# Performance work log

Hardware: AMD Instinct MI355X
Metric: run time of the kernel (lower is better)

Reference implementation:

```python
import jax, jax.numpy as jnp
import numpy as np

NUM_LEVELS = 12
LEVEL_DIM = 2
BASE_RES = 16
DESIRED_RES = 8192
LOG2_HASH = 21
PRIMES = (1, 2654435761, 805459861)


def _level_specs(D):
    # torch-ngp GridEncoder table layout: per-level (offset, size, scale, res, use_hash)
    f = (DESIRED_RES / BASE_RES) ** (1.0 / (NUM_LEVELS - 1))
    specs = []
    offset = 0
    for l in range(NUM_LEVELS):
        scale = BASE_RES * (f ** l) - 1.0
        res = int(np.ceil(scale)) + 1
        dense = (res + 1) ** D  # align_corners=False -> stride uses res+1
        params = min(2 ** LOG2_HASH, dense)
        params = int(np.ceil(params / 8) * 8)
        specs.append((offset, params, scale, res, dense > 2 ** LOG2_HASH))
        offset += params
    return specs, offset


def grid_encode(x, table, D):
    # x: [N, D] in [-1, 1]; table: [T, LEVEL_DIM]. Returns [N, NUM_LEVELS*LEVEL_DIM].
    x01 = (x + 1.0) * 0.5  # (inputs + bound) / (2*bound), bound=1
    specs, _ = _level_specs(D)
    feats = []
    for (off, hsize, scale, res, use_hash) in specs:
        pos = x01 * scale + 0.5  # align_corners=False
        pg_f = jnp.floor(pos)
        frac = pos - pg_f          # [N, D]
        pg = pg_f.astype(jnp.uint32)
        acc = jnp.zeros((x.shape[0], LEVEL_DIM), dtype=table.dtype)
        for c in range(2 ** D):  # 4 or 8 corners, static unroll
            w = None
            idx = jnp.zeros((x.shape[0],), dtype=jnp.uint32)
            stride = 1
            for d in range(D):
                bit = (c >> d) & 1
                coord = pg[:, d] + jnp.uint32(bit)
                wd = frac[:, d] if bit else (1.0 - frac[:, d])
                w = wd if w is None else w * wd
                if use_hash:
                    idx = idx ^ (coord * jnp.uint32(PRIMES[d]))  # uint32 wraparound xor-hash
                else:
                    idx = idx + coord * jnp.uint32(stride)
                    stride *= (res + 1)
            gidx = (idx % jnp.uint32(hsize)).astype(jnp.int32) + off
            acc = acc + w[:, None] * table[gidx]
        feats.append(acc)
    return jnp.concatenate(feats, axis=-1)


def mlp(feat, w1, b1, w2, b2):
    h = jax.nn.relu(feat @ w1 + b1)
    return h @ w2 + b2


def setup_inputs() -> dict:
    key = jax.random.key(0)
    ks = jax.random.split(key, 16)
    B, P = 4096, 1000
    line = jax.random.uniform(ks[0], (B, 2), dtype=jnp.float32)
    line_points = jax.random.uniform(ks[1], (B, P, 3), dtype=jnp.float32)
    gt_o = jax.random.uniform(ks[2], (B, P), dtype=jnp.float32)
    _, tot2 = _level_specs(2)
    _, tot3 = _level_specs(3)
    table_conf = jax.random.uniform(ks[3], (tot2, LEVEL_DIM), jnp.float32, -1e-4, 1e-4)
    table_op = jax.random.uniform(ks[4], (tot3, LEVEL_DIM), jnp.float32, -1e-4, 1e-4)
    F = NUM_LEVELS * LEVEL_DIM  # 24
    w1_c = jax.random.normal(ks[5], (F, 64), jnp.float32) * 0.1
    b1_c = jnp.zeros((64,), jnp.float32)
    w2_c = jax.random.normal(ks[6], (64, 1), jnp.float32) * 0.1
    b2_c = jnp.zeros((1,), jnp.float32)
    w1_o = jax.random.normal(ks[7], (F, 64), jnp.float32) * 0.1
    b1_o = jnp.zeros((64,), jnp.float32)
    w2_o = jax.random.normal(ks[8], (64, 1), jnp.float32) * 0.1
    b2_o = jnp.zeros((1,), jnp.float32)
    return {"line": line, "line_points": line_points, "gt_o": gt_o,
            "table_conf": table_conf, "w1_c": w1_c, "b1_c": b1_c, "w2_c": w2_c, "b2_c": b2_c,
            "table_op": table_op, "w1_o": w1_o, "b1_o": b1_o, "w2_o": w2_o, "b2_o": b2_o}


def reference(line, line_points, gt_o, table_conf, w1_c, b1_c, w2_c, b2_c,
              table_op, w1_o, b1_o, w2_o, b2_o):
    B, P, _ = line_points.shape
    pts = line_points.reshape(B * P, 3)
    feat_o = grid_encode(pts, table_op, 3)             # [B*P, 24]
    opacity = mlp(feat_o, w1_o, b1_o, w2_o, b2_o).reshape(B, P)  # squeeze(2)
    feat_c = grid_encode(line, table_conf, 2)          # [B, 24]
    confidence = mlp(feat_c, w1_c, b1_c, w2_c, b2_c)[:, 0]       # squeeze(1)
    loss1 = jnp.abs(opacity - gt_o)
    col_w = jnp.where(jnp.arange(P) < 500, 4.0 / 3.0, 2.0 / 3.0).astype(loss1.dtype)
    loss1 = loss1 * col_w[None, :]
    loss = jnp.exp(-confidence) * loss1.mean(axis=1) + confidence
    return loss.mean()
```

## Files before the change

kernel.cpp:

```cpp
#include <hip/hip_runtime.h>
#include <hip/hip_bf16.h>
#include <math.h>

#define NLEV 12
#define B_LINES 4096
#define P_PTS 1000
#define FP8_SCALE 65536.0f
#define FP8_ISCALE (1.0f / 65536.0f)

typedef unsigned short ushort_t;
typedef __attribute__((ext_vector_type(8))) short short8_t;
typedef __attribute__((ext_vector_type(4))) float f32x4;

struct LevelSpec {
    unsigned off;
    unsigned mask;
    float    scale;
    unsigned R;
};
struct Specs { LevelSpec L[NLEV]; };
struct HashScales { float s[8]; };

static unsigned compute_specs(int D, Specs* sp) {
    double f = pow(8192.0 / 16.0, 1.0 / 11.0);
    unsigned offset = 0;
    for (int l = 0; l < NLEV; ++l) {
        double scale = 16.0 * pow(f, (double)l) - 1.0;
        int res = (int)ceil(scale) + 1;
        unsigned long long dense = 1ull;
        for (int d = 0; d < D; ++d) dense *= (unsigned long long)(res + 1);
        unsigned long long params = dense > (1ull << 21) ? (1ull << 21) : dense;
        params = ((params + 7ull) / 8ull) * 8ull;
        sp->L[l].off   = offset;
        sp->L[l].mask  = (unsigned)params - 1u;
        sp->L[l].scale = (float)scale;
        sp->L[l].R     = (unsigned)(res + 1);
        offset += (unsigned)params;
    }
    return offset;
}


__device__ __forceinline__ float block_reduce_256(float v) {
    __shared__ float red[256];
    int tid = threadIdx.x;
    red[tid] = v;
    __syncthreads();
    #pragma unroll
    for (int s = 128; s >= 1; s >>= 1) {
        if (tid < s) red[tid] += red[tid + s];
        __syncthreads();
    }
    return red[0];
}

__device__ __forceinline__ unsigned short f32_to_bf16_bits(float f) {
    unsigned u = __float_as_uint(f);
    unsigned r = (u + 0x7fffu + ((u >> 16) & 1u)) >> 16;
    return (unsigned short)r;
}

__device__ __forceinline__ float mlp_24_64_1(const float feat[24],
        const float* __restrict__ w1, const float* __restrict__ b1,
        const float* __restrict__ w2, const float* __restrict__ b2) {
    float o = b2[0];
    #pragma unroll
    for (int half = 0; half < 2; ++half) {
        float h[32];
        #pragma unroll
        for (int j = 0; j < 32; ++j) h[j] = b1[half * 32 + j];
        #pragma unroll
        for (int k = 0; k < 24; ++k) {
            float fv = feat[k];
            #pragma unroll
            for (int j = 0; j < 32; ++j)
                h[j] = fmaf(fv, w1[k * 64 + half * 32 + j], h[j]);
        }
        #pragma unroll
        for (int j = 0; j < 32; ++j)
            o = fmaf(fmaxf(h[j], 0.f), w2[half * 32 + j], o);
    }
    return o;
}

__global__ void __launch_bounds__(256) convert_kernel(
        const float2* __restrict__ in, ushort_t* __restrict__ out, int n) {
    int i = blockIdx.x * 256 + threadIdx.x;
    if (i >= n) return;
    float2 v = in[i];
    int p = __builtin_amdgcn_cvt_pk_fp8_f32(v.x * FP8_SCALE, v.y * FP8_SCALE,
                                            0, false);
    out[i] = (ushort_t)(p & 0xffff);
}

__global__ void __launch_bounds__(256) enc_dense_kernel(
        const float* __restrict__ pts, int pbase, int npts,
        const ushort_t* __restrict__ tabq,
        __hip_bfloat162* __restrict__ feats,
        Specs sp) {
    int i = blockIdx.x * 256 + threadIdx.x;
    if (i >= npts) return;
    int gp = pbase + i;
    float x0 = (pts[3 * gp + 0] + 1.f) * 0.5f;
    float x1 = (pts[3 * gp + 1] + 1.f) * 0.5f;
    float x2 = (pts[3 * gp + 2] + 1.f) * 0.5f;
    #pragma unroll
    for (int l = 0; l < 4; ++l) {
        const LevelSpec L = sp.L[l];
        float p0 = x0 * L.scale + 0.5f;
        float p1 = x1 * L.scale + 0.5f;
        float p2 = x2 * L.scale + 0.5f;
        float f0 = floorf(p0), f1 = floorf(p1), f2 = floorf(p2);
        float r0 = p0 - f0, r1 = p1 - f1, r2 = p2 - f2;
        float u0 = 1.f - r0, u1 = 1.f - r1, u2 = 1.f - r2;
        unsigned g0 = (unsigned)f0, g1 = (unsigned)f1, g2 = (unsigned)f2;
        const ushort_t* __restrict__ base = tabq + L.off;
        unsigned R = L.R, R2 = R * R;
        unsigned y0 = g1 * R, y1 = y0 + R;
        unsigned z0 = g2 * R2, z1 = z0 + R2;
        int t[8];
        #pragma unroll
        for (int c = 0; c < 8; ++c) {
            unsigned idx = (g0 + ((c & 1) ? 1u : 0u))
                         + ((c & 2) ? y1 : y0) + ((c & 4) ? z1 : z0);
            t[c] = (int)base[idx];
        }
        float a0 = 0.f, a1 = 0.f;
        #pragma unroll
        for (int c = 0; c < 8; ++c) {
            float w = ((c & 1) ? r0 : u0) * ((c & 2) ? r1 : u1)
                    * ((c & 4) ? r2 : u2);
            a0 = fmaf(w, __builtin_amdgcn_cvt_f32_fp8(t[c], 0), a0);
            a1 = fmaf(w, __builtin_amdgcn_cvt_f32_fp8(t[c], 1), a1);
        }
        __hip_bfloat162 o;
        o.x = __float2bfloat16(a0 * FP8_ISCALE);
        o.y = __float2bfloat16(a1 * FP8_ISCALE);
        feats[(size_t)l * npts + i] = o;
    }
}

__global__ void __launch_bounds__(256) enc_hash_all_kernel(
        const float* __restrict__ pts, int pbase, int npts,
        const ushort_t* __restrict__ tabq, unsigned hash_off0,
        HashScales hs,
        __hip_bfloat162* __restrict__ feats) {
    const int lev = blockIdx.x & 7;
    const int i = (blockIdx.x >> 3) * 256 + threadIdx.x;
    if (i >= npts) return;
    float scale = hs.s[0];
    #pragma unroll
    for (int k = 1; k < 8; ++k) if (lev == k) scale = hs.s[k];
    const ushort_t* __restrict__ base =
        tabq + hash_off0 + ((unsigned)lev << 21);
    const unsigned m = (1u << 21) - 1u;

    int gp = pbase + i;
    float x0 = (pts[3 * gp + 0] + 1.f) * 0.5f;
    float x1 = (pts[3 * gp + 1] + 1.f) * 0.5f;
    float x2 = (pts[3 * gp + 2] + 1.f) * 0.5f;
    float p0 = x0 * scale + 0.5f;
    float p1 = x1 * scale + 0.5f;
    float p2 = x2 * scale + 0.5f;
    float f0 = floorf(p0), f1 = floorf(p1), f2 = floorf(p2);
    float r0 = p0 - f0, r1 = p1 - f1, r2 = p2 - f2;
    float u0 = 1.f - r0, u1 = 1.f - r1, u2 = 1.f - r2;
    unsigned g0 = (unsigned)f0, g1 = (unsigned)f1, g2 = (unsigned)f2;
    unsigned y0 = g1 * 2654435761u, y1 = y0 + 2654435761u;
    unsigned z0 = g2 * 805459861u,  z1 = z0 + 805459861u;
    int t[8];
    #pragma unroll
    for (int c = 0; c < 8; ++c) {
        unsigned h = (g0 + ((c & 1) ? 1u : 0u))
                   ^ ((c & 2) ? y1 : y0) ^ ((c & 4) ? z1 : z0);
        t[c] = (int)base[h & m];
    }
    float a0 = 0.f, a1 = 0.f;
    #pragma unroll
    for (int c = 0; c < 8; ++c) {
        float w = ((c & 1) ? r0 : u0) * ((c & 2) ? r1 : u1)
                * ((c & 4) ? r2 : u2);
        a0 = fmaf(w, __builtin_amdgcn_cvt_f32_fp8(t[c], 0), a0);
        a1 = fmaf(w, __builtin_amdgcn_cvt_f32_fp8(t[c], 1), a1);
    }
    __hip_bfloat162 o;
    o.x = __float2bfloat16(a0 * FP8_ISCALE);
    o.y = __float2bfloat16(a1 * FP8_ISCALE);
    feats[(size_t)(4 + lev) * npts + i] = o;
}

__global__ void __launch_bounds__(256) mlp_loss_mfma_kernel(
        const unsigned* __restrict__ feats, int npts,
        const float* __restrict__ gt, int line0,
        const float* __restrict__ w1, const float* __restrict__ b1,
        const float* __restrict__ w2, const float* __restrict__ b2,
        float* __restrict__ S) {
    const int line_local = blockIdx.x;
    const int tid  = threadIdx.x;
    const int wave = tid >> 6;
    const int lane = tid & 63;
    const int c = lane & 15;
    const int g = lane >> 4;

    short8_t bfrag[4];
    #pragma unroll
    for (int nb = 0; nb < 4; ++nb) {
        #pragma unroll
        for (int i = 0; i < 8; ++i) {
            int k = g * 8 + i;
            float v = (k < 24) ? w1[k * 64 + nb * 16 + c] : 0.f;
            bfrag[nb][i] = (short)f32_to_bf16_bits(v);
        }
    }
    float b1v[4], w2v[4];
    #pragma unroll
    for (int nb = 0; nb < 4; ++nb) {
        b1v[nb] = b1[nb * 16 + c];
        w2v[nb] = w2[nb * 16 + c];
    }
    const float b2v = b2[0];

    const size_t lbase = (size_t)line_local * P_PTS;
    float lsum = 0.f;

    for (int it = 0; it < 16; ++it) {
        const int base16 = it * 64 + wave * 16;
        int prow = base16 + c;
        int pcl  = prow < P_PTS ? prow : P_PTS - 1;
        size_t pidx = lbase + (size_t)pcl;
        union { unsigned u[4]; short8_t v; } a;
        if (g < 3) {
            #pragma unroll
            for (int s = 0; s < 4; ++s)
                a.u[s] = feats[(size_t)(g * 4 + s) * npts + pidx];
        } else {
            a.u[0] = 0u; a.u[1] = 0u; a.u[2] = 0u; a.u[3] = 0u;
        }
        f32x4 acc[4];
        #pragma unroll
        for (int nb = 0; nb < 4; ++nb) {
            f32x4 ci = {b1v[nb], b1v[nb], b1v[nb], b1v[nb]};
            acc[nb] = __builtin_amdgcn_mfma_f32_16x16x32_bf16(
                a.v, bfrag[nb], ci, 0, 0, 0);
        }
        float part[4];
        #pragma unroll
        for (int r = 0; r < 4; ++r) {
            float s = fmaxf(acc[0][r], 0.f) * w2v[0];
            s = fmaf(fmaxf(acc[1][r], 0.f), w2v[1], s);
            s = fmaf(fmaxf(acc[2][r], 0.f), w2v[2], s);
            s = fmaf(fmaxf(acc[3][r], 0.f), w2v[3], s);
            part[r] = s;
        }
        #pragma unroll
        for (int off = 1; off < 16; off <<= 1) {
            #pragma unroll
            for (int r = 0; r < 4; ++r)
                part[r] += __shfl_xor(part[r], off);
        }
        if (c < 4) {
            int p = base16 + g * 4 + c;
            if (p < P_PTS) {
                float op = part[c] + b2v;
                float gv = gt[(size_t)(line0 + line_local) * P_PTS + p];
                float cw = (p < 500) ? (float)(4.0 / 3.0) : (float)(2.0 / 3.0);
                lsum += fabsf(op - gv) * cw;
            }
        }
    }
    float tot = block_reduce_256(lsum);
    if (tid == 0) S[line0 + line_local] = tot;
}

__global__ void __launch_bounds__(256) opacity_mono_kernel(
        const float* __restrict__ pts, const float* __restrict__ gt,
        const float2* __restrict__ tab,
        const float* __restrict__ w1, const float* __restrict__ b1,
        const float* __restrict__ w2, const float* __restrict__ b2,
        float* __restrict__ S, Specs sp) {
    const int b = blockIdx.x;
    const int tid = threadIdx.x;
    float lsum = 0.f;
    for (int p = tid; p < P_PTS; p += 256) {
        const int i = b * P_PTS + p;
        float x0 = (pts[3 * i + 0] + 1.f) * 0.5f;
        float x1 = (pts[3 * i + 1] + 1.f) * 0.5f;
        float x2 = (pts[3 * i + 2] + 1.f) * 0.5f;
        float feat[24];
        #pragma unroll
        for (int l = 0; l < NLEV; ++l) {
            const LevelSpec L = sp.L[l];
            float p0 = x0 * L.scale + 0.5f;
            float p1 = x1 * L.scale + 0.5f;
            float p2 = x2 * L.scale + 0.5f;
            float f0 = floorf(p0), f1 = floorf(p1), f2 = floorf(p2);
            float r0 = p0 - f0, r1 = p1 - f1, r2 = p2 - f2;
            float u0 = 1.f - r0, u1 = 1.f - r1, u2 = 1.f - r2;
            unsigned g0 = (unsigned)f0, g1 = (unsigned)f1, g2 = (unsigned)f2;
            float a0 = 0.f, a1 = 0.f;
            if (l >= 4) {
                unsigned y0 = g1 * 2654435761u, y1 = y0 + 2654435761u;
                unsigned z0 = g2 * 805459861u,  z1 = z0 + 805459861u;
                unsigned m = L.mask;
                #pragma unroll
                for (int c = 0; c < 8; ++c) {
                    unsigned h = (g0 + ((c & 1) ? 1u : 0u))
                               ^ ((c & 2) ? y1 : y0) ^ ((c & 4) ? z1 : z0);
                    float2 t = tab[L.off + (h & m)];
                    float w = ((c & 1) ? r0 : u0) * ((c & 2) ? r1 : u1)
                            * ((c & 4) ? r2 : u2);
                    a0 = fmaf(w, t.x, a0); a1 = fmaf(w, t.y, a1);
                }
            } else {
                unsigned R = L.R, R2 = R * R;
                unsigned y0 = g1 * R, y1 = y0 + R;
                unsigned z0 = g2 * R2, z1 = z0 + R2;
                #pragma unroll
                for (int c = 0; c < 8; ++c) {
                    unsigned idx = (g0 + ((c & 1) ? 1u : 0u))
                                 + ((c & 2) ? y1 : y0) + ((c & 4) ? z1 : z0);
                    float2 t = tab[L.off + idx];
                    float w = ((c & 1) ? r0 : u0) * ((c & 2) ? r1 : u1)
                            * ((c & 4) ? r2 : u2);
                    a0 = fmaf(w, t.x, a0); a1 = fmaf(w, t.y, a1);
                }
            }
            feat[2 * l] = a0; feat[2 * l + 1] = a1;
        }
        float op = mlp_24_64_1(feat, w1, b1, w2, b2);
        float cw = (p < 500) ? (float)(4.0 / 3.0) : (float)(2.0 / 3.0);
        lsum += fabsf(op - gt[i]) * cw;
    }
    float tot = block_reduce_256(lsum);
    if (tid == 0) S[b] = tot;
}

__global__ void __launch_bounds__(256) conf_kernel(
        const float* __restrict__ line, const float2* __restrict__ tab,
        const float* __restrict__ w1, const float* __restrict__ b1,
        const float* __restrict__ w2, const float* __restrict__ b2,
        const float* __restrict__ S, float* __restrict__ partial, Specs sp) {
    const int b = blockIdx.x * 256 + threadIdx.x;
    float x0 = (line[2 * b + 0] + 1.f) * 0.5f;
    float x1 = (line[2 * b + 1] + 1.f) * 0.5f;
    float feat[24];
    #pragma unroll
    for (int l = 0; l < NLEV; ++l) {
        const unsigned off = sp.L[l].off;
        const float scale = sp.L[l].scale;
        float p0 = x0 * scale + 0.5f;
        float p1 = x1 * scale + 0.5f;
        float f0 = floorf(p0), f1 = floorf(p1);
        float r0 = p0 - f0, r1 = p1 - f1;
        float u0 = 1.f - r0, u1 = 1.f - r1;
        unsigned g0 = (unsigned)f0, g1 = (unsigned)f1;
        unsigned idx0, idx1, idx2, idx3;
        if (l >= 8) {
            const unsigned mask = sp.L[l].mask;
            unsigned a1 = g1 * 2654435761u, bb1 = a1 + 2654435761u;
            idx0 = (g0 ^ a1) & mask;
            idx1 = ((g0 + 1u) ^ a1) & mask;
            idx2 = (g0 ^ bb1) & mask;
            idx3 = ((g0 + 1u) ^ bb1) & mask;
        } else {
            const unsigned R = sp.L[l].R;
            unsigned a1 = g1 * R, bb1 = a1 + R;
            idx0 = g0 + a1; idx1 = g0 + 1u + a1;
            idx2 = g0 + bb1; idx3 = g0 + 1u + bb1;
        }
        float2 t0 = tab[off + idx0], t1 = tab[off + idx1];
        float2 t2 = tab[off + idx2], t3 = tab[off + idx3];
        float w0 = u0 * u1, w1c = r0 * u1, w2c = u0 * r1, w3 = r0 * r1;
        feat[2 * l]     = w0 * t0.x + w1c * t1.x + w2c * t2.x + w3 * t3.x;
        feat[2 * l + 1] = w0 * t0.y + w1c * t1.y + w2c * t2.y + w3 * t3.y;
    }
    float conf = mlp_24_64_1(feat, w1, b1, w2, b2);
    float term = expf(-conf) * (S[b] * (1.0f / (float)P_PTS)) + conf;
    float tot = block_reduce_256(term);
    if (threadIdx.x == 0) partial[blockIdx.x] = tot;
}

__global__ void final_kernel(const float* __restrict__ partial,
                             float* __restrict__ out) {
    if (threadIdx.x == 0) {
        float s = 0.f;
        for (int i = 0; i < 16; ++i) s += partial[i];
        out[0] = s * (1.0f / (float)B_LINES);
    }
}


extern "C" void kernel_launch(void* const* d_in, const int* in_sizes, int n_in,
                              void* d_out, int out_size, void* d_ws, size_t ws_size,
                              hipStream_t stream) {
    const float* line    = (const float*)d_in[0];
    const float* pts     = (const float*)d_in[1];
    const float* gt      = (const float*)d_in[2];
    const float* table_c = (const float*)d_in[3];
    const float* w1_c    = (const float*)d_in[4];
    const float* b1_c    = (const float*)d_in[5];
    const float* w2_c    = (const float*)d_in[6];
    const float* b2_c    = (const float*)d_in[7];
    const float* table_o = (const float*)d_in[8];
    const float* w1_o    = (const float*)d_in[9];
    const float* b1_o    = (const float*)d_in[10];
    const float* w2_o    = (const float*)d_in[11];
    const float* b2_o    = (const float*)d_in[12];
    (void)in_sizes; (void)n_in; (void)out_size;

    Specs sp3, sp2;
    unsigned tot3 = compute_specs(3, &sp3);
    compute_specs(2, &sp2);

    size_t tabB = (((size_t)tot3 * 2) + 255) & ~(size_t)255;
    size_t head = tabB + (size_t)B_LINES * 4 + 64;
    head = (head + 63) & ~(size_t)63;
    long max_lines = 0;
    if (ws_size > head + 64)
        max_lines = (long)((ws_size - head - 64) / ((size_t)P_PTS * 12 * 4));

    float* S       = (float*)((char*)d_ws + tabB);
    float* partial = S + B_LINES;

    if (max_lines >= 64) {
        ushort_t* tabq = (ushort_t*)d_ws;
        __hip_bfloat162* featbuf = (__hip_bfloat162*)((char*)d_ws + head);

        int chunk_lines = (int)(max_lines < B_LINES ? max_lines : B_LINES);
        int nch = (B_LINES + chunk_lines - 1) / chunk_lines;

        HashScales hs;
        for (int k = 0; k < 8; ++k) hs.s[k] = sp3.L[4 + k].scale;
        const unsigned hash_off0 = sp3.L[4].off;

        convert_kernel<<<((int)tot3 + 255) / 256, 256, 0, stream>>>(
            (const float2*)table_o, tabq, (int)tot3);

        for (int ch = 0; ch < nch; ++ch) {
            int line0 = ch * chunk_lines;
            int lines = B_LINES - line0 < chunk_lines ? B_LINES - line0
                                                      : chunk_lines;
            int npts = lines * P_PTS;
            int pbase = line0 * P_PTS;
            int nblk = (npts + 255) / 256;
            enc_dense_kernel<<<nblk, 256, 0, stream>>>(
                pts, pbase, npts, tabq, featbuf, sp3);
            enc_hash_all_kernel<<<nblk * 8, 256, 0, stream>>>(
                pts, pbase, npts, tabq, hash_off0, hs, featbuf);
            mlp_loss_mfma_kernel<<<lines, 256, 0, stream>>>(
                (const unsigned*)featbuf, npts, gt, line0,
                w1_o, b1_o, w2_o, b2_o, S);
        }
    } else {
        opacity_mono_kernel<<<B_LINES, 256, 0, stream>>>(
            pts, gt, (const float2*)table_o, w1_o, b1_o, w2_o, b2_o, S, sp3);
    }

    conf_kernel<<<16, 256, 0, stream>>>(
        line, (const float2*)table_c, w1_c, b1_c, w2_c, b2_c, S, partial, sp2);
    final_kernel<<<1, 64, 0, stream>>>(partial, (float*)d_out);
}
```

Before: 1.577 ms.

## Use persistent grid-stride hash encoding with two points per thread and nontemporal I/O

The hash-level encoder now launches a fixed 256 blocks per level and grid-strides over points. Each thread processes two points per iteration and issues all 16 table gathers before interpolating, which raises memory-level parallelism. Streaming loads of points and the fp32 table, and stores of features and the fp8 table, switch to nontemporal hints so they pollute the cache less and leave room for the random table gathers. Clamped indices for out-of-range tail points add some redundant work, and the fixed grid size may underfill or overfill the GPU depending on chunk size.

```diff
diff --git a/kernel.cpp b/kernel.cpp
--- a/kernel.cpp
+++ b/kernel.cpp
@@ -7,6 +7,7 @@
 #define P_PTS 1000
 #define FP8_SCALE 65536.0f
 #define FP8_ISCALE (1.0f / 65536.0f)
+#define NBLK_PER_LEV 256
 
 typedef unsigned short ushort_t;
 typedef __attribute__((ext_vector_type(8))) short short8_t;
@@ -60,6 +61,14 @@
     return (unsigned short)r;
 }
 
+__device__ __forceinline__ void store_nt_feat(__hip_bfloat162* p,
+                                              float a0, float a1) {
+    union { __hip_bfloat162 b; unsigned u; } cv;
+    cv.b.x = __float2bfloat16(a0 * FP8_ISCALE);
+    cv.b.y = __float2bfloat16(a1 * FP8_ISCALE);
+    __builtin_nontemporal_store(cv.u, (unsigned*)p);
+}
+
 __device__ __forceinline__ float mlp_24_64_1(const float feat[24],
         const float* __restrict__ w1, const float* __restrict__ b1,
         const float* __restrict__ w2, const float* __restrict__ b2) {
@@ -87,10 +96,12 @@
         const float2* __restrict__ in, ushort_t* __restrict__ out, int n) {
     int i = blockIdx.x * 256 + threadIdx.x;
     if (i >= n) return;
-    float2 v = in[i];
+    float2 v;
+    v.x = __builtin_nontemporal_load(&in[i].x);
+    v.y = __builtin_nontemporal_load(&in[i].y);
     int p = __builtin_amdgcn_cvt_pk_fp8_f32(v.x * FP8_SCALE, v.y * FP8_SCALE,
                                             0, false);
-    out[i] = (ushort_t)(p & 0xffff);
+    __builtin_nontemporal_store((ushort_t)(p & 0xffff), &out[i]);
 }
 
 __global__ void __launch_bounds__(256) enc_dense_kernel(
@@ -101,9 +112,9 @@
     int i = blockIdx.x * 256 + threadIdx.x;
     if (i >= npts) return;
     int gp = pbase + i;
-    float x0 = (pts[3 * gp + 0] + 1.f) * 0.5f;
-    float x1 = (pts[3 * gp + 1] + 1.f) * 0.5f;
-    float x2 = (pts[3 * gp + 2] + 1.f) * 0.5f;
+    float x0 = (__builtin_nontemporal_load(pts + 3 * gp + 0) + 1.f) * 0.5f;
+    float x1 = (__builtin_nontemporal_load(pts + 3 * gp + 1) + 1.f) * 0.5f;
+    float x2 = (__builtin_nontemporal_load(pts + 3 * gp + 2) + 1.f) * 0.5f;
     #pragma unroll
     for (int l = 0; l < 4; ++l) {
         const LevelSpec L = sp.L[l];
@@ -133,11 +144,47 @@
             a0 = fmaf(w, __builtin_amdgcn_cvt_f32_fp8(t[c], 0), a0);
             a1 = fmaf(w, __builtin_amdgcn_cvt_f32_fp8(t[c], 1), a1);
         }
-        __hip_bfloat162 o;
-        o.x = __float2bfloat16(a0 * FP8_ISCALE);
-        o.y = __float2bfloat16(a1 * FP8_ISCALE);
-        feats[(size_t)l * npts + i] = o;
-    }
+        store_nt_feat(&feats[(size_t)l * npts + i], a0, a1);
+    }
+}
+
+struct HashPt { unsigned h[8]; float r0, r1, r2; };
+
+__device__ __forceinline__ HashPt hash_addrs(
+        const float* __restrict__ pts, int gp, float scale, unsigned m) {
+    float x0 = (__builtin_nontemporal_load(pts + 3 * gp + 0) + 1.f) * 0.5f;
+    float x1 = (__builtin_nontemporal_load(pts + 3 * gp + 1) + 1.f) * 0.5f;
+    float x2 = (__builtin_nontemporal_load(pts + 3 * gp + 2) + 1.f) * 0.5f;
+    float p0 = x0 * scale + 0.5f;
+    float p1 = x1 * scale + 0.5f;
+    float p2 = x2 * scale + 0.5f;
+    float f0 = floorf(p0), f1 = floorf(p1), f2 = floorf(p2);
+    HashPt o;
+    o.r0 = p0 - f0; o.r1 = p1 - f1; o.r2 = p2 - f2;
+    unsigned g0 = (unsigned)f0, g1 = (unsigned)f1, g2 = (unsigned)f2;
+    unsigned y0 = g1 * 2654435761u, y1 = y0 + 2654435761u;
+    unsigned z0 = g2 * 805459861u,  z1 = z0 + 805459861u;
+    #pragma unroll
+    for (int c = 0; c < 8; ++c) {
+        unsigned h = (g0 + ((c & 1) ? 1u : 0u))
+                   ^ ((c & 2) ? y1 : y0) ^ ((c & 4) ? z1 : z0);
+        o.h[c] = h & m;
+    }
+    return o;
+}
+
+__device__ __forceinline__ void interp_store(
+        const int t[8], const HashPt& hp, __hip_bfloat162* dst) {
+    float u0 = 1.f - hp.r0, u1 = 1.f - hp.r1, u2 = 1.f - hp.r2;
+    float a0 = 0.f, a1 = 0.f;
+    #pragma unroll
+    for (int c = 0; c < 8; ++c) {
+        float w = ((c & 1) ? hp.r0 : u0) * ((c & 2) ? hp.r1 : u1)
+                * ((c & 4) ? hp.r2 : u2);
+        a0 = fmaf(w, __builtin_amdgcn_cvt_f32_fp8(t[c], 0), a0);
+        a1 = fmaf(w, __builtin_amdgcn_cvt_f32_fp8(t[c], 1), a1);
+    }
+    store_nt_feat(dst, a0, a1);
 }
 
 __global__ void __launch_bounds__(256) enc_hash_all_kernel(
@@ -146,47 +193,33 @@
         HashScales hs,
         __hip_bfloat162* __restrict__ feats) {
     const int lev = blockIdx.x & 7;
-    const int i = (blockIdx.x >> 3) * 256 + threadIdx.x;
-    if (i >= npts) return;
+    const int bpl = blockIdx.x >> 3;
+    const int tid = threadIdx.x;
     float scale = hs.s[0];
     #pragma unroll
     for (int k = 1; k < 8; ++k) if (lev == k) scale = hs.s[k];
     const ushort_t* __restrict__ base =
         tabq + hash_off0 + ((unsigned)lev << 21);
     const unsigned m = (1u << 21) - 1u;
-
-    int gp = pbase + i;
-    float x0 = (pts[3 * gp + 0] + 1.f) * 0.5f;
-    float x1 = (pts[3 * gp + 1] + 1.f) * 0.5f;
-    float x2 = (pts[3 * gp + 2] + 1.f) * 0.5f;
-    float p0 = x0 * scale + 0.5f;
-    float p1 = x1 * scale + 0.5f;
-    float p2 = x2 * scale + 0.5f;
-    float f0 = floorf(p0), f1 = floorf(p1), f2 = floorf(p2);
-    float r0 = p0 - f0, r1 = p1 - f1, r2 = p2 - f2;
-    float u0 = 1.f - r0, u1 = 1.f - r1, u2 = 1.f - r2;
-    unsigned g0 = (unsigned)f0, g1 = (unsigned)f1, g2 = (unsigned)f2;
-    unsigned y0 = g1 * 2654435761u, y1 = y0 + 2654435761u;
-    unsigned z0 = g2 * 805459861u,  z1 = z0 + 805459861u;
-    int t[8];
-    #pragma unroll
-    for (int c = 0; c < 8; ++c) {
-        unsigned h = (g0 + ((c & 1) ? 1u : 0u))
-                   ^ ((c & 2) ? y1 : y0) ^ ((c & 4) ? z1 : z0);
-        t[c] = (int)base[h & m];
-    }
-    float a0 = 0.f, a1 = 0.f;
-    #pragma unroll
-    for (int c = 0; c < 8; ++c) {
-        float w = ((c & 1) ? r0 : u0) * ((c & 2) ? r1 : u1)
-                * ((c & 4) ? r2 : u2);
-        a0 = fmaf(w, __builtin_amdgcn_cvt_f32_fp8(t[c], 0), a0);
-        a1 = fmaf(w, __builtin_amdgcn_cvt_f32_fp8(t[c], 1), a1);
-    }
-    __hip_bfloat162 o;
-    o.x = __float2bfloat16(a0 * FP8_ISCALE);
-    o.y = __float2bfloat16(a1 * FP8_ISCALE);
-    feats[(size_t)(4 + lev) * npts + i] = o;
+    __hip_bfloat162* __restrict__ slab = feats + (size_t)(4 + lev) * npts;
+
+    const int stride = NBLK_PER_LEV * 512;
+    for (int p0 = bpl * 512; p0 < npts; p0 += stride) {
+        int iA = p0 + tid;
+        int iB = iA + 256;
+        bool vA = iA < npts, vB = iB < npts;
+        int icA = vA ? iA : npts - 1;
+        int icB = vB ? iB : npts - 1;
+        HashPt hA = hash_addrs(pts, pbase + icA, scale, m);
+        HashPt hB = hash_addrs(pts, pbase + icB, scale, m);
+        int tA[8], tB[8];
+        #pragma unroll
+        for (int c = 0; c < 8; ++c) tA[c] = (int)base[hA.h[c]];
+        #pragma unroll
+        for (int c = 0; c < 8; ++c) tB[c] = (int)base[hB.h[c]];
+        if (vA) interp_store(tA, hA, slab + iA);
+        if (vB) interp_store(tB, hB, slab + iB);
+    }
 }
 
 __global__ void __launch_bounds__(256) mlp_loss_mfma_kernel(
@@ -445,7 +478,7 @@
             int nblk = (npts + 255) / 256;
             enc_dense_kernel<<<nblk, 256, 0, stream>>>(
                 pts, pbase, npts, tabq, featbuf, sp3);
-            enc_hash_all_kernel<<<nblk * 8, 256, 0, stream>>>(
+            enc_hash_all_kernel<<<NBLK_PER_LEV * 8, 256, 0, stream>>>(
                 pts, pbase, npts, tabq, hash_off0, hs, featbuf);
             mlp_loss_mfma_kernel<<<lines, 256, 0, stream>>>(
                 (const unsigned*)featbuf, npts, gt, line0,
```

Result: faster. 1.486 ms (-5.8%).
